# Kernel tuning notes

Measured on AMD Instinct MI355X. Metric: run time of the kernel, lower is better.

## Reference

```python
import jax, jax.numpy as jnp
import numpy as np
import math

HEAD_DIM = 128
N_HEADS = 32
N_KV_HEADS = 8
HIDDEN = 4096
ROPE_BASE = 10000.0


def _rope_cos_sin(position_ids):
    # inv_freq: [D/2]
    inv_freq = 1.0 / (ROPE_BASE ** (jnp.arange(0, HEAD_DIM, 2, dtype=jnp.float32) / HEAD_DIM))
    freqs = position_ids.astype(jnp.float32)[..., None] * inv_freq  # [B,S,D/2]
    emb = jnp.concatenate([freqs, freqs], axis=-1)  # [B,S,D]
    return jnp.cos(emb), jnp.sin(emb)


def _rotate_half(x):
    x1, x2 = jnp.split(x, 2, axis=-1)
    return jnp.concatenate([-x2, x1], axis=-1)


def setup_inputs() -> dict:
    key = jax.random.key(0)
    ks = jax.random.split(key, 5)
    B, S = 1, 2048
    inp = {
        "hidden_states": jax.random.normal(ks[0], (B, S, HIDDEN), dtype=jnp.float32),
        "position_ids": jnp.arange(B * S, dtype=jnp.int32).reshape(B, S),
        "Wq": jax.random.normal(ks[1], (HIDDEN, N_HEADS * HEAD_DIM), dtype=jnp.float32) * 0.02,
        "Wk": jax.random.normal(ks[2], (HIDDEN, N_KV_HEADS * HEAD_DIM), dtype=jnp.float32) * 0.02,
        "Wv": jax.random.normal(ks[3], (HIDDEN, N_KV_HEADS * HEAD_DIM), dtype=jnp.float32) * 0.02,
        "Wo": jax.random.normal(ks[4], (N_HEADS * HEAD_DIM, HIDDEN), dtype=jnp.float32) * 0.02,
    }
    return inp


def reference(hidden_states, position_ids, Wq, Wk, Wv, Wo):
    B, S, _ = hidden_states.shape
    G = N_HEADS // N_KV_HEADS

    q = (hidden_states @ Wq).reshape(B, S, N_HEADS, HEAD_DIM).transpose(0, 2, 1, 3)      # [B,H,S,D]
    k = (hidden_states @ Wk).reshape(B, S, N_KV_HEADS, HEAD_DIM).transpose(0, 2, 1, 3)   # [B,Hkv,S,D]
    v = (hidden_states @ Wv).reshape(B, S, N_KV_HEADS, HEAD_DIM).transpose(0, 2, 1, 3)

    cos, sin = _rope_cos_sin(position_ids)          # [B,S,D]
    cos = cos[:, None, :, :]                         # [B,1,S,D]
    sin = sin[:, None, :, :]
    q = q * cos + _rotate_half(q) * sin
    k = k * cos + _rotate_half(k) * sin

    # GQA head expansion (repeat_interleave over head dim)
    k = jnp.repeat(k, G, axis=1)                     # [B,H,S,D]
    v = jnp.repeat(v, G, axis=1)

    scale = 1.0 / math.sqrt(HEAD_DIM)
    scores = jnp.einsum("bhqd,bhkd->bhqk", q, k) * scale  # [B,H,S,S]
    causal = jnp.triu(jnp.full((S, S), -jnp.inf, dtype=scores.dtype), k=1)
    scores = scores + causal[None, None]
    probs = jax.nn.softmax(scores.astype(jnp.float32), axis=-1).astype(q.dtype)
    ctx = jnp.einsum("bhqk,bhkd->bhqd", probs, v)    # [B,H,S,D]
    ctx = ctx.transpose(0, 2, 1, 3).reshape(B, S, N_HEADS * HEAD_DIM)
    return ctx @ Wo
```

## Files before the change

kernel.cpp:

```cpp
#include <hip/hip_runtime.h>
#include <hip/hip_bf16.h>
#include <math.h>

#define SEQ 2048
#define NHEADS 32
#define NKVH 8
#define HD 128
#define HIDDEN 4096

typedef unsigned short u16;
typedef unsigned int u32;
typedef __attribute__((ext_vector_type(8))) __bf16 bf16x8;
typedef __attribute__((ext_vector_type(4))) float f32x4;
typedef __attribute__((ext_vector_type(16))) float f32x16;
typedef __attribute__((ext_vector_type(4))) u16 u16x4;
typedef __attribute__((ext_vector_type(4))) u32 u32x4;

__device__ __forceinline__ u16 f2bf(float f) {
  u32 u = __builtin_bit_cast(u32, f);
  u32 r = (u + 0x7fffu + ((u >> 16) & 1u)) >> 16;
  return (u16)r;
}
__device__ __forceinline__ float bf2f(u16 h) {
  return __builtin_bit_cast(float, ((u32)h) << 16);
}
__device__ __forceinline__ void gload_lds16(const void* g, void* l) {
  __builtin_amdgcn_global_load_lds(
      (const __attribute__((address_space(1))) u32*)g,
      (__attribute__((address_space(3))) u32*)l, 16, 0, 0);
}

#define BAR __builtin_amdgcn_s_barrier()
#define PRIO1 __builtin_amdgcn_s_setprio(1)
#define PRIO0 __builtin_amdgcn_s_setprio(0)
#define VMW(n) asm volatile("s_waitcnt vmcnt(" #n ")" ::: "memory")

__global__ void __launch_bounds__(256) conv_f2b_vec(const float* __restrict__ in,
                                                    u16* __restrict__ out, const int n) {
  const int i = (blockIdx.x * 256 + threadIdx.x) * 4;
  if (i >= n) return;
  const float4 v = *(const float4*)(in + i);
  u16x4 o;
  o.x = f2bf(v.x); o.y = f2bf(v.y); o.z = f2bf(v.z); o.w = f2bf(v.w);
  *(u16x4*)(out + i) = o;
}

__global__ void __launch_bounds__(256) trans_f2b(const float* __restrict__ in,
                                                 u16* __restrict__ out, const int R, const int C) {
  __shared__ float tile[32][33];
  const int c0 = blockIdx.x * 32, r0 = blockIdx.y * 32;
  const int tx = threadIdx.x & 31, ty = threadIdx.x >> 5;
#pragma unroll
  for (int i = 0; i < 4; ++i)
    tile[ty + i * 8][tx] = in[(size_t)(r0 + ty + i * 8) * C + c0 + tx];
  __syncthreads();
#pragma unroll
  for (int i = 0; i < 4; ++i)
    out[(size_t)(c0 + ty + i * 8) * R + r0 + tx] = f2bf(tile[tx][ty + i * 8]);
}

__global__ void __launch_bounds__(256) trans_b2b(const u16* __restrict__ in,
                                                 u16* __restrict__ out, const int R, const int C) {
  __shared__ u16 tile[32][34];
  const int c0 = blockIdx.x * 32, r0 = blockIdx.y * 32;
  const int tx = threadIdx.x & 31, ty = threadIdx.x >> 5;
#pragma unroll
  for (int i = 0; i < 4; ++i)
    tile[ty + i * 8][tx] = in[(size_t)(r0 + ty + i * 8) * C + c0 + tx];
  __syncthreads();
#pragma unroll
  for (int i = 0; i < 4; ++i)
    out[(size_t)(c0 + ty + i * 8) * R + r0 + tx] = tile[tx][ty + i * 8];
}

__global__ void __launch_bounds__(256) rope_ip(u16* __restrict__ x, const int* __restrict__ pos,
                                               const int lognh, const float oscale) {
  const int idx = blockIdx.x * 256 + threadIdx.x;
  const int j = idx & 63;
  const int hh = (idx >> 6) & ((1 << lognh) - 1);
  const int s = idx >> (6 + lognh);
  if (s >= SEQ) return;
  const float p = (float)pos[s];
  const float invf = __expf((float)j * -0.14391156831212787f);
  const float ang = p * invf;
  const float c = cosf(ang), sn = sinf(ang);
  u16* bp = x + ((size_t)s << (7 + lognh)) + hh * 128 + j;
  const float x1 = bf2f(bp[0]), x2 = bf2f(bp[64]);
  bp[0] = f2bf((x1 * c - x2 * sn) * oscale);
  bp[64] = f2bf((x2 * c + x1 * sn) * oscale);
}

template <int MH, int NH>
__device__ __forceinline__ void mfq32(f32x16 (&acc)[4][2], const bf16x8 (&afr)[2][4],
                                      const bf16x8 (&b)[4]) {
#pragma unroll
  for (int f = 0; f < 2; ++f)
#pragma unroll
    for (int ks = 0; ks < 4; ++ks)
      acc[MH * 2 + f][NH] = __builtin_amdgcn_mfma_f32_32x32x16_bf16(
          afr[f][ks], b[ks], acc[MH * 2 + f][NH], 0, 0, 0);
}

__global__ void __launch_bounds__(512, 2) gemm8p32(
    const u16* __restrict__ A, const u16* __restrict__ B0q, const u16* __restrict__ B1q,
    const u16* __restrict__ B2q, u16* __restrict__ C0, u16* __restrict__ C1,
    u16* __restrict__ C2, const float* __restrict__ Wsrc, u16* __restrict__ Wdst) {
  __shared__ u16 As[2][2][128 * 64];
  __shared__ u16 Bs[2][2][128 * 64];
  const int t = threadIdx.x;
  const int flat = blockIdx.x;
  const int swz = (flat & 7) * 32 + (flat >> 3);

  if (swz >= 192) {
    const int wid = swz - 192;
    float* tf = (float*)&As[0][0][0];
    const int tx = t & 63, ty = t >> 6;
    const int r0 = wid * 64;
    for (int ct = 0; ct < 64; ++ct) {
      const int c0 = ct * 64;
#pragma unroll
      for (int i = 0; i < 8; ++i)
        tf[(ty + i * 8) * 65 + tx] = Wsrc[(size_t)(r0 + ty + i * 8) * 4096 + c0 + tx];
      __syncthreads();
#pragma unroll
      for (int i = 0; i < 8; ++i)
        Wdst[(size_t)(c0 + ty + i * 8) * 4096 + r0 + tx] = f2bf(tf[tx * 65 + ty + i * 8]);
      __syncthreads();
    }
    return;
  }

  const int lane = t & 63, w = t >> 6;
  const int wr = w >> 2, wc = w & 3;
  const int l31 = lane & 31, l5 = lane >> 5;

  int bxt = swz % 24;
  const int byt = swz / 24;
  const u16* Bp; u16* Cw; int Nn;
  if (bxt < 16) { Bp = B0q; Cw = C0; Nn = 4096; }
  else if (bxt < 20) { bxt -= 16; Bp = B1q; Cw = C1; Nn = 1024; }
  else { bxt -= 20; Bp = B2q; Cw = C2; Nn = 1024; }
  const int row0 = byt * 256, col0 = bxt * 256;

  auto stageA = [&](int buf, int half, int tile) {
#pragma unroll
    for (int g = 0; g < 2; ++g) {
      const int o = (g * 512 + t) * 16;
      const int ridx = o >> 7;
      const int slot = (o >> 4) & 7;
      const int gr = (ridx >> 6) * 128 + half * 64 + (ridx & 63);
      gload_lds16(A + (size_t)(row0 + gr) * 4096 + (tile << 6) + ((slot ^ (ridx & 7)) << 3),
                  (char*)&As[buf][half][0] + o);
    }
  };
  auto stageB = [&](int buf, int half, int tile) {
#pragma unroll
    for (int g = 0; g < 2; ++g) {
      const int o = (g * 512 + t) * 16;
      const int ridx = o >> 7;
      const int slot = (o >> 4) & 7;
      const int gn = (ridx >> 5) * 64 + half * 32 + (ridx & 31);
      gload_lds16(Bp + (size_t)(col0 + gn) * 4096 + (tile << 6) + ((slot ^ (ridx & 7)) << 3),
                  (char*)&Bs[buf][half][0] + o);
    }
  };

  bf16x8 afr[2][4], bf0[4], bf1[4];
  auto loadA32 = [&](int buf, int half) {
#pragma unroll
    for (int f = 0; f < 2; ++f)
#pragma unroll
      for (int ks = 0; ks < 4; ++ks) {
        const int idx = wr * 64 + f * 32 + l31;
        const int slot = ks * 2 + l5;
        afr[f][ks] = *(const bf16x8*)((const char*)&As[buf][half][0] + idx * 128 +
                                      ((slot ^ (idx & 7)) << 4));
      }
  };
  auto loadB32 = [&](int buf, int half, bf16x8 (&dst)[4]) {
#pragma unroll
    for (int ks = 0; ks < 4; ++ks) {
      const int idx = wc * 32 + l31;
      const int slot = ks * 2 + l5;
      dst[ks] = *(const bf16x8*)((const char*)&Bs[buf][half][0] + idx * 128 +
                                 ((slot ^ (idx & 7)) << 4));
    }
  };

  f32x16 acc[4][2];
#pragma unroll
  for (int m_ = 0; m_ < 4; ++m_)
#pragma unroll
    for (int n_ = 0; n_ < 2; ++n_)
#pragma unroll
      for (int e = 0; e < 16; ++e) acc[m_][n_][e] = 0.f;

  const int nit = (4096 >> 6) >> 1;

  stageA(0, 0, 0); stageA(0, 1, 0); stageB(0, 0, 0); stageB(0, 1, 0);
  stageA(1, 0, 1); stageB(1, 1, 1);
  VMW(4);
  BAR;

  for (int i = 0; i < nit; ++i) {
    const int tb = 2 * i;
    const bool g2 = (i + 1 < nit);
    loadA32(0, 0); loadB32(0, 0, bf0);
    stageA(1, 1, tb + 1);
    BAR; PRIO1; mfq32<0, 0>(acc, afr, bf0); PRIO0; BAR;
    loadB32(0, 1, bf1);
    stageB(1, 0, tb + 1);
    BAR; PRIO1; mfq32<0, 1>(acc, afr, bf1); PRIO0; BAR;
    loadA32(0, 1);
    if (g2) stageA(0, 0, tb + 2);
    BAR; PRIO1; mfq32<1, 1>(acc, afr, bf1); PRIO0; BAR;
    if (g2) stageB(0, 1, tb + 2);
    BAR; PRIO1; mfq32<1, 0>(acc, afr, bf0); PRIO0;
    if (g2) { VMW(4); } else { VMW(0); }
    BAR;
    loadA32(1, 0); loadB32(1, 0, bf0);
    if (g2) stageA(0, 1, tb + 2);
    BAR; PRIO1; mfq32<0, 0>(acc, afr, bf0); PRIO0; BAR;
    loadB32(1, 1, bf1);
    if (g2) stageB(0, 0, tb + 2);
    BAR; PRIO1; mfq32<0, 1>(acc, afr, bf1); PRIO0; BAR;
    loadA32(1, 1);
    if (g2) stageA(1, 0, tb + 3);
    BAR; PRIO1; mfq32<1, 1>(acc, afr, bf1); PRIO0; BAR;
    if (g2) stageB(1, 1, tb + 3);
    BAR; PRIO1; mfq32<1, 0>(acc, afr, bf0); PRIO0;
    if (g2) { VMW(4); } else { VMW(0); }
    BAR;
  }

#pragma unroll
  for (int am = 0; am < 4; ++am)
#pragma unroll
    for (int an = 0; an < 2; ++an) {
      const int colb = col0 + wc * 64 + an * 32 + l31;
#pragma unroll
      for (int q = 0; q < 4; ++q) {
        const int rowb = row0 + wr * 128 + am * 32 + q * 8 + l5 * 4;
#pragma unroll
        for (int rr = 0; rr < 4; ++rr)
          Cw[(size_t)(rowb + rr) * Nn + colb] = f2bf(acc[am][an][q * 4 + rr]);
      }
    }
}

template <int MH, int NH>
__device__ __forceinline__ void mfq16(f32x4 (&acc)[4][4], const bf16x8 (&af)[2][2],
                                      const bf16x8 (&b)[2][2]) {
#pragma unroll
  for (int f = 0; f < 2; ++f)
#pragma unroll
    for (int e = 0; e < 2; ++e)
#pragma unroll
      for (int ks = 0; ks < 2; ++ks)
        acc[MH * 2 + f][NH * 2 + e] = __builtin_amdgcn_mfma_f32_16x16x32_bf16(
            af[f][ks], b[e][ks], acc[MH * 2 + f][NH * 2 + e], 0, 0, 0);
}

__global__ void __launch_bounds__(512, 2) gemm8p16(
    const u16* __restrict__ A, const u16* __restrict__ B, float* __restrict__ C) {
  __shared__ u16 As[2][2][64 * 64];
  __shared__ u16 Bs[2][2][128 * 64];
  const int t = threadIdx.x;
  const int lane = t & 63, w = t >> 6;
  const int wr = w >> 2, wc = w & 3;
  const int l15 = lane & 15, l4 = lane >> 4;

  const int flat = blockIdx.x;
  const int swz = (flat & 7) * 32 + (flat >> 3);
  const int bxt = swz & 15, byt = swz >> 4;
  const int row0 = byt * 128, col0 = bxt * 256;

  auto stageA = [&](int buf, int half, int tile) {
    const int o = t * 16;
    const int ridx = o >> 7;
    const int slot = (o >> 4) & 7;
    const int gr = (ridx >> 5) * 64 + half * 32 + (ridx & 31);
    gload_lds16(A + (size_t)(row0 + gr) * 4096 + (tile << 6) + ((slot ^ (ridx & 7)) << 3),
                (char*)&As[buf][half][0] + o);
  };
  auto stageB = [&](int buf, int half, int tile) {
#pragma unroll
    for (int g = 0; g < 2; ++g) {
      const int o = (g * 512 + t) * 16;
      const int ridx = o >> 7;
      const int slot = (o >> 4) & 7;
      const int gn = (ridx >> 5) * 64 + half * 32 + (ridx & 31);
      gload_lds16(B + (size_t)(col0 + gn) * 4096 + (tile << 6) + ((slot ^ (ridx & 7)) << 3),
                  (char*)&Bs[buf][half][0] + o);
    }
  };

  bf16x8 af[2][2], bf0[2][2], bf1[2][2];
  auto loadA = [&](int buf, int half) {
#pragma unroll
    for (int f = 0; f < 2; ++f)
#pragma unroll
      for (int ks = 0; ks < 2; ++ks) {
        const int idx = wr * 32 + f * 16 + l15;
        const int slot = ks * 4 + l4;
        af[f][ks] = *(const bf16x8*)((const char*)&As[buf][half][0] + idx * 128 +
                                     ((slot ^ (idx & 7)) << 4));
      }
  };
  auto loadB = [&](int buf, int half, bf16x8 (&dst)[2][2]) {
#pragma unroll
    for (int e = 0; e < 2; ++e)
#pragma unroll
      for (int ks = 0; ks < 2; ++ks) {
        const int idx = wc * 32 + e * 16 + l15;
        const int slot = ks * 4 + l4;
        dst[e][ks] = *(const bf16x8*)((const char*)&Bs[buf][half][0] + idx * 128 +
                                      ((slot ^ (idx & 7)) << 4));
      }
  };

  f32x4 acc[4][4];
#pragma unroll
  for (int m_ = 0; m_ < 4; ++m_)
#pragma unroll
    for (int n_ = 0; n_ < 4; ++n_) acc[m_][n_] = f32x4{0.f, 0.f, 0.f, 0.f};

  const int nit = (4096 >> 6) >> 1;

  stageA(0, 0, 0); stageA(0, 1, 0); stageB(0, 0, 0); stageB(0, 1, 0);
  stageA(1, 0, 1); stageB(1, 1, 1);
  VMW(3);
  BAR;

  for (int i = 0; i < nit; ++i) {
    const int tb = 2 * i;
    const bool g2 = (i + 1 < nit);
    loadA(0, 0); loadB(0, 0, bf0);
    stageA(1, 1, tb + 1);
    BAR; PRIO1; mfq16<0, 0>(acc, af, bf0); PRIO0; BAR;
    loadB(0, 1, bf1);
    stageB(1, 0, tb + 1);
    BAR; PRIO1; mfq16<0, 1>(acc, af, bf1); PRIO0; BAR;
    loadA(0, 1);
    if (g2) stageA(0, 0, tb + 2);
    BAR; PRIO1; mfq16<1, 1>(acc, af, bf1); PRIO0; BAR;
    if (g2) stageB(0, 1, tb + 2);
    BAR; PRIO1; mfq16<1, 0>(acc, af, bf0); PRIO0;
    if (g2) { VMW(3); } else { VMW(0); }
    BAR;
    loadA(1, 0); loadB(1, 0, bf0);
    if (g2) stageA(0, 1, tb + 2);
    BAR; PRIO1; mfq16<0, 0>(acc, af, bf0); PRIO0; BAR;
    loadB(1, 1, bf1);
    if (g2) stageB(0, 0, tb + 2);
    BAR; PRIO1; mfq16<0, 1>(acc, af, bf1); PRIO0; BAR;
    loadA(1, 1);
    if (g2) stageA(1, 0, tb + 3);
    BAR; PRIO1; mfq16<1, 1>(acc, af, bf1); PRIO0; BAR;
    if (g2) stageB(1, 1, tb + 3);
    BAR; PRIO1; mfq16<1, 0>(acc, af, bf0); PRIO0;
    if (g2) { VMW(3); } else { VMW(0); }
    BAR;
  }

#pragma unroll
  for (int am = 0; am < 4; ++am) {
    const int rowb = row0 + wr * 64 + (am >> 1) * 32 + (am & 1) * 16 + l4 * 4;
#pragma unroll
    for (int an = 0; an < 4; ++an) {
      const int colb = col0 + wc * 64 + (an >> 1) * 32 + (an & 1) * 16 + l15;
#pragma unroll
      for (int r = 0; r < 4; ++r)
        C[(size_t)(rowb + r) * 4096 + colb] = acc[am][an][r];
    }
  }
}

__device__ __forceinline__ void stage_kv(const u16* __restrict__ k, const u16* __restrict__ vt,
                                         const int kvh, const int kv0, u16* KsB, u16* VsB,
                                         const int t) {
#pragma unroll
  for (int i = 0; i < 4; ++i) {
    const int o = (i * 256 + t) * 16;
    const int row = o >> 8;
    const int slot = (o >> 4) & 15;
    gload_lds16(k + (size_t)(kv0 + row) * (NKVH * HD) + kvh * HD + ((slot ^ (row & 7)) << 3),
                (char*)KsB + o);
  }
#pragma unroll
  for (int i = 0; i < 4; ++i) {
    const int o = (i * 256 + t) * 16;
    const int row = o >> 7;
    const int slot = (o >> 4) & 7;
    gload_lds16(vt + (size_t)(kvh * HD + row) * SEQ + kv0 + ((slot ^ (row & 7)) << 3),
                (char*)VsB + o);
  }
}

__global__ void __launch_bounds__(256) attn_fwd(const u16* __restrict__ q, const u16* __restrict__ k,
                                                const u16* __restrict__ vt, u16* __restrict__ ctx) {
  __shared__ u16 Ks[2][64 * 128];
  __shared__ u16 Vs[2][128 * 64];
  const int t = threadIdx.x, lane = t & 63, w = t >> 6;
  const int h = blockIdx.x;
  const int qb = (int)gridDim.y - 1 - (int)blockIdx.y;
  const int kvh = h >> 2;
  const int q0 = qb * 64;
  const int sq_base = q0 + w * 16;
  const int l15 = lane & 15, l4 = lane >> 4;
  const int sq_abs = sq_base + l15;

  bf16x8 qf[4];
  {
    const u16* qp = q + (size_t)sq_abs * (NHEADS * HD) + h * HD + l4 * 8;
#pragma unroll
    for (int kb = 0; kb < 4; ++kb) qf[kb] = *(const bf16x8*)(qp + kb * 32);
  }
  f32x4 po[8];
#pragma unroll
  for (int i = 0; i < 8; ++i) po[i] = f32x4{0.f, 0.f, 0.f, 0.f};
  float mrow = -1e30f;
  float lrow = 0.f;

  const int nb = qb + 1;
  stage_kv(k, vt, kvh, 0, Ks[0], Vs[0], t);
  __syncthreads();
  int cur = 0;

  for (int b = 0; b < nb; ++b) {
    if (b + 1 < nb) stage_kv(k, vt, kvh, (b + 1) * 64, Ks[cur ^ 1], Vs[cur ^ 1], t);

    f32x4 st[4];
#pragma unroll
    for (int c = 0; c < 4; ++c) st[c] = f32x4{0.f, 0.f, 0.f, 0.f};
#pragma unroll
    for (int c = 0; c < 4; ++c) {
      const int row = c * 16 + l15;
#pragma unroll
      for (int kb = 0; kb < 4; ++kb) {
        const int slot = kb * 4 + l4;
        bf16x8 bk = *(const bf16x8*)((const char*)Ks[cur] + row * 256 + ((slot ^ (row & 7)) << 4));
        st[c] = __builtin_amdgcn_mfma_f32_16x16x32_bf16(bk, qf[kb], st[c], 0, 0, 0);
      }
    }

    if (b == nb - 1) {
#pragma unroll
      for (int c = 0; c < 4; ++c)
#pragma unroll
        for (int r = 0; r < 4; ++r) {
          const int sk = b * 64 + c * 16 + l4 * 4 + r;
          if (sk > sq_abs) st[c][r] = -1e30f;
        }
    }

    float rmax = -3e38f;
#pragma unroll
    for (int c = 0; c < 4; ++c)
      rmax = fmaxf(rmax, fmaxf(fmaxf(st[c][0], st[c][1]), fmaxf(st[c][2], st[c][3])));
    rmax = fmaxf(rmax, __shfl_xor(rmax, 16, 64));
    rmax = fmaxf(rmax, __shfl_xor(rmax, 32, 64));

    const bool skip = __all(rmax <= mrow + 8.f);
    const float mnew = skip ? mrow : fmaxf(mrow, rmax);

    float rs = 0.f;
#pragma unroll
    for (int c = 0; c < 4; ++c) {
      const float e0 = exp2f(st[c][0] - mnew), e1 = exp2f(st[c][1] - mnew);
      const float e2 = exp2f(st[c][2] - mnew), e3 = exp2f(st[c][3] - mnew);
      st[c][0] = e0; st[c][1] = e1; st[c][2] = e2; st[c][3] = e3;
      rs += (e0 + e1) + (e2 + e3);
    }
    rs += __shfl_xor(rs, 16, 64);
    rs += __shfl_xor(rs, 32, 64);

    if (!skip) {
      const float alpha = exp2f(mrow - mnew);
      mrow = mnew;
      lrow = lrow * alpha + rs;
      float av[4];
#pragma unroll
      for (int r = 0; r < 4; ++r) av[r] = __shfl(alpha, l4 * 4 + r, 16);
#pragma unroll
      for (int db = 0; db < 8; ++db)
#pragma unroll
        for (int r = 0; r < 4; ++r) po[db][r] *= av[r];
    } else {
      lrow += rs;
    }

    u32 pk[4][2];
#pragma unroll
    for (int c = 0; c < 4; ++c) {
      pk[c][0] = (u32)f2bf(st[c][0]) | ((u32)f2bf(st[c][1]) << 16);
      pk[c][1] = (u32)f2bf(st[c][2]) | ((u32)f2bf(st[c][3]) << 16);
    }
    const int src01 = l15 + ((lane & 16) << 1);
    const int src23 = src01 + 16;
    const bool lo = (lane & 32) == 0;
#pragma unroll
    for (int kb2 = 0; kb2 < 2; ++kb2) {
      const int c0 = kb2 * 2, c1 = c0 + 1;
      const u32 a0 = (u32)__shfl((int)pk[c0][0], src01, 64);
      const u32 a1 = (u32)__shfl((int)pk[c0][1], src01, 64);
      const u32 a2 = (u32)__shfl((int)pk[c0][0], src23, 64);
      const u32 a3 = (u32)__shfl((int)pk[c0][1], src23, 64);
      const u32 b0 = (u32)__shfl((int)pk[c1][0], src01, 64);
      const u32 b1 = (u32)__shfl((int)pk[c1][1], src01, 64);
      const u32 b2 = (u32)__shfl((int)pk[c1][0], src23, 64);
      const u32 b3 = (u32)__shfl((int)pk[c1][1], src23, 64);
      u32x4 wq;
      wq.x = lo ? a0 : b0;
      wq.y = lo ? a1 : b1;
      wq.z = lo ? a2 : b2;
      wq.w = lo ? a3 : b3;
      const bf16x8 pa = __builtin_bit_cast(bf16x8, wq);
#pragma unroll
      for (int db = 0; db < 8; ++db) {
        const int vrow = db * 16 + l15;
        const int pslot = kb2 * 4 + l4;
        bf16x8 bv = *(const bf16x8*)((const char*)Vs[cur] + vrow * 128 + ((pslot ^ (vrow & 7)) << 4));
        po[db] = __builtin_amdgcn_mfma_f32_16x16x32_bf16(pa, bv, po[db], 0, 0, 0);
      }
    }
    __syncthreads();
    cur ^= 1;
  }

  float rl[4];
#pragma unroll
  for (int r = 0; r < 4; ++r) rl[r] = 1.f / __shfl(lrow, l4 * 4 + r, 16);
#pragma unroll
  for (int db = 0; db < 8; ++db)
#pragma unroll
    for (int r = 0; r < 4; ++r) {
      const int sq = sq_base + l4 * 4 + r;
      const int d = db * 16 + l15;
      ctx[(size_t)sq * (NHEADS * HD) + h * HD + d] = f2bf(po[db][r] * rl[r]);
    }
}

extern "C" void kernel_launch(void* const* d_in, const int* in_sizes, int n_in,
                              void* d_out, int out_size, void* d_ws, size_t ws_size,
                              hipStream_t stream) {
  const float* hs = (const float*)d_in[0];
  const int* pos = (const int*)d_in[1];
  const float* Wq = (const float*)d_in[2];
  const float* Wk = (const float*)d_in[3];
  const float* Wv = (const float*)d_in[4];
  const float* Wo = (const float*)d_in[5];

  u16* ws = (u16*)d_ws;
  u16* Xb = ws;
  u16* Wqt = Xb + (size_t)2048 * 4096;
  u16* Wkt = Wqt + (size_t)4096 * 4096;
  u16* Wvt = Wkt + (size_t)1024 * 4096;
  u16* Wot = Wvt + (size_t)1024 * 4096;
  u16* qb = Wot + (size_t)4096 * 4096;
  u16* kb = qb + (size_t)2048 * 4096;
  u16* vb = kb + (size_t)2048 * 1024;
  u16* vtb = vb + (size_t)2048 * 1024;
  u16* ctx = vtb + (size_t)1024 * 2048;
  const size_t need = ((size_t)(ctx - ws) + (size_t)2048 * 4096) * 2;
  if (ws_size < need) return;

  conv_f2b_vec<<<8192, 256, 0, stream>>>(hs, Xb, 2048 * 4096);
  trans_f2b<<<dim3(128, 128), 256, 0, stream>>>(Wq, Wqt, 4096, 4096);
  trans_f2b<<<dim3(32, 128), 256, 0, stream>>>(Wk, Wkt, 4096, 1024);
  trans_f2b<<<dim3(32, 128), 256, 0, stream>>>(Wv, Wvt, 4096, 1024);

  gemm8p32<<<256, 512, 0, stream>>>(Xb, Wqt, Wkt, Wvt, qb, kb, vb, Wo, Wot);

  const float qscale = 0.08838834764831845f * 1.44269504088896340f;
  rope_ip<<<16384, 256, 0, stream>>>(qb, pos, 5, qscale);
  rope_ip<<<4096, 256, 0, stream>>>(kb, pos, 3, 1.0f);

  trans_b2b<<<dim3(32, 64), 256, 0, stream>>>(vb, vtb, 2048, 1024);

  attn_fwd<<<dim3(32, 32), 256, 0, stream>>>(qb, kb, vtb, ctx);

  gemm8p16<<<256, 512, 0, stream>>>(ctx, Wot, (float*)d_out);
}
```

Measured before the change: 351.5 us.

## Restructure GEMM main loops for register-prefetched fragments and fuse prep kernels

Both 8-phase GEMM kernels now double-buffer the register fragments for A and B (even/odd sets). Each phase loads the fragments for the next MFMA block while the current one runs, and the last iteration is peeled into a separate tail. The goal is to hide LDS read latency behind MFMA work and drop the per-iteration conditional staging. Separately, the four input-preparation launches (hidden-state conversion plus three weight transposes) are merged into one kernel with 64x64 transpose tiles, which cuts launch overhead. The cost is higher register pressure and the extra vmcnt waits now placed in every phase.

```diff
diff --git a/kernel.cpp b/kernel.cpp
--- a/kernel.cpp
+++ b/kernel.cpp
@@ -35,42 +35,35 @@
 #define PRIO0 __builtin_amdgcn_s_setprio(0)
 #define VMW(n) asm volatile("s_waitcnt vmcnt(" #n ")" ::: "memory")
 
-__global__ void __launch_bounds__(256) conv_f2b_vec(const float* __restrict__ in,
-                                                    u16* __restrict__ out, const int n) {
-  const int i = (blockIdx.x * 256 + threadIdx.x) * 4;
-  if (i >= n) return;
-  const float4 v = *(const float4*)(in + i);
-  u16x4 o;
-  o.x = f2bf(v.x); o.y = f2bf(v.y); o.z = f2bf(v.z); o.w = f2bf(v.w);
-  *(u16x4*)(out + i) = o;
-}
-
-__global__ void __launch_bounds__(256) trans_f2b(const float* __restrict__ in,
-                                                 u16* __restrict__ out, const int R, const int C) {
-  __shared__ float tile[32][33];
-  const int c0 = blockIdx.x * 32, r0 = blockIdx.y * 32;
-  const int tx = threadIdx.x & 31, ty = threadIdx.x >> 5;
-#pragma unroll
-  for (int i = 0; i < 4; ++i)
-    tile[ty + i * 8][tx] = in[(size_t)(r0 + ty + i * 8) * C + c0 + tx];
+__global__ void __launch_bounds__(256) prep_all(
+    const float* __restrict__ hs, u16* __restrict__ Xb,
+    const float* __restrict__ Wq, u16* __restrict__ Wqt,
+    const float* __restrict__ Wk, u16* __restrict__ Wkt,
+    const float* __restrict__ Wv, u16* __restrict__ Wvt) {
+  const int bid = blockIdx.x;
+  if (bid < 8192) {
+    const int i = (bid * 256 + threadIdx.x) * 4;
+    const float4 v = *(const float4*)(hs + i);
+    u16x4 o;
+    o.x = f2bf(v.x); o.y = f2bf(v.y); o.z = f2bf(v.z); o.w = f2bf(v.w);
+    *(u16x4*)(Xb + i) = o;
+    return;
+  }
+  __shared__ float tile[64][65];
+  const float* src; u16* dst; int C, lc, tb;
+  const int b2 = bid - 8192;
+  if (b2 < 4096) { src = Wq; dst = Wqt; C = 4096; lc = 6; tb = b2; }
+  else if (b2 < 5120) { src = Wk; dst = Wkt; C = 1024; lc = 4; tb = b2 - 4096; }
+  else { src = Wv; dst = Wvt; C = 1024; lc = 4; tb = b2 - 5120; }
+  const int r0 = (tb >> lc) * 64, c0 = (tb & ((1 << lc) - 1)) * 64;
+  const int tx = threadIdx.x & 63, ty = threadIdx.x >> 6;
+#pragma unroll
+  for (int j = 0; j < 16; ++j)
+    tile[ty + j * 4][tx] = src[(size_t)(r0 + ty + j * 4) * C + c0 + tx];
   __syncthreads();
 #pragma unroll
-  for (int i = 0; i < 4; ++i)
-    out[(size_t)(c0 + ty + i * 8) * R + r0 + tx] = f2bf(tile[tx][ty + i * 8]);
-}
-
-__global__ void __launch_bounds__(256) trans_b2b(const u16* __restrict__ in,
-                                                 u16* __restrict__ out, const int R, const int C) {
-  __shared__ u16 tile[32][34];
-  const int c0 = blockIdx.x * 32, r0 = blockIdx.y * 32;
-  const int tx = threadIdx.x & 31, ty = threadIdx.x >> 5;
-#pragma unroll
-  for (int i = 0; i < 4; ++i)
-    tile[ty + i * 8][tx] = in[(size_t)(r0 + ty + i * 8) * C + c0 + tx];
-  __syncthreads();
-#pragma unroll
-  for (int i = 0; i < 4; ++i)
-    out[(size_t)(c0 + ty + i * 8) * R + r0 + tx] = tile[tx][ty + i * 8];
+  for (int j = 0; j < 16; ++j)
+    dst[(size_t)(c0 + ty + j * 4) * 4096 + r0 + tx] = f2bf(tile[tx][ty + j * 4]);
 }
 
 __global__ void __launch_bounds__(256) rope_ip(u16* __restrict__ x, const int* __restrict__ pos,
@@ -90,6 +83,20 @@
   bp[64] = f2bf((x2 * c + x1 * sn) * oscale);
 }
 
+__global__ void __launch_bounds__(256) trans_b2b(const u16* __restrict__ in,
+                                                 u16* __restrict__ out, const int R, const int C) {
+  __shared__ u16 tile[32][34];
+  const int c0 = blockIdx.x * 32, r0 = blockIdx.y * 32;
+  const int tx = threadIdx.x & 31, ty = threadIdx.x >> 5;
+#pragma unroll
+  for (int i = 0; i < 4; ++i)
+    tile[ty + i * 8][tx] = in[(size_t)(r0 + ty + i * 8) * C + c0 + tx];
+  __syncthreads();
+#pragma unroll
+  for (int i = 0; i < 4; ++i)
+    out[(size_t)(c0 + ty + i * 8) * R + r0 + tx] = tile[tx][ty + i * 8];
+}
+
 template <int MH, int NH>
 __device__ __forceinline__ void mfq32(f32x16 (&acc)[4][2], const bf16x8 (&afr)[2][4],
                                       const bf16x8 (&b)[4]) {
@@ -165,17 +172,15 @@
     }
   };
 
-  bf16x8 afr[2][4], bf0[4], bf1[4];
-  auto loadA32 = [&](int buf, int half) {
-#pragma unroll
-    for (int f = 0; f < 2; ++f)
-#pragma unroll
-      for (int ks = 0; ks < 4; ++ks) {
-        const int idx = wr * 64 + f * 32 + l31;
-        const int slot = ks * 2 + l5;
-        afr[f][ks] = *(const bf16x8*)((const char*)&As[buf][half][0] + idx * 128 +
-                                      ((slot ^ (idx & 7)) << 4));
-      }
+  bf16x8 aE[2][4], aO[2][4], bX[4], bY[4];
+  auto loadAf = [&](int buf, int half, int f, bf16x8 (&dst)[4]) {
+#pragma unroll
+    for (int ks = 0; ks < 4; ++ks) {
+      const int idx = wr * 64 + f * 32 + l31;
+      const int slot = ks * 2 + l5;
+      dst[ks] = *(const bf16x8*)((const char*)&As[buf][half][0] + idx * 128 +
+                                 ((slot ^ (idx & 7)) << 4));
+    }
   };
   auto loadB32 = [&](int buf, int half, bf16x8 (&dst)[4]) {
 #pragma unroll
@@ -197,41 +202,61 @@
 
   const int nit = (4096 >> 6) >> 1;
 
-  stageA(0, 0, 0); stageA(0, 1, 0); stageB(0, 0, 0); stageB(0, 1, 0);
-  stageA(1, 0, 1); stageB(1, 1, 1);
-  VMW(4);
+  stageA(0, 0, 0); stageB(0, 0, 0); stageA(0, 1, 0); stageB(0, 1, 0);
+  stageA(1, 0, 1); stageB(1, 0, 1); stageA(1, 1, 1); stageB(1, 1, 1);
+  VMW(6);
   BAR;
-
-  for (int i = 0; i < nit; ++i) {
+  loadAf(0, 0, 0, aE[0]); loadAf(0, 0, 1, aE[1]); loadB32(0, 0, bX);
+  BAR;
+
+  for (int i = 0; i < nit - 1; ++i) {
     const int tb = 2 * i;
-    const bool g2 = (i + 1 < nit);
-    loadA32(0, 0); loadB32(0, 0, bf0);
-    stageA(1, 1, tb + 1);
-    BAR; PRIO1; mfq32<0, 0>(acc, afr, bf0); PRIO0; BAR;
-    loadB32(0, 1, bf1);
-    stageB(1, 0, tb + 1);
-    BAR; PRIO1; mfq32<0, 1>(acc, afr, bf1); PRIO0; BAR;
-    loadA32(0, 1);
-    if (g2) stageA(0, 0, tb + 2);
-    BAR; PRIO1; mfq32<1, 1>(acc, afr, bf1); PRIO0; BAR;
-    if (g2) stageB(0, 1, tb + 2);
-    BAR; PRIO1; mfq32<1, 0>(acc, afr, bf0); PRIO0;
-    if (g2) { VMW(4); } else { VMW(0); }
-    BAR;
-    loadA32(1, 0); loadB32(1, 0, bf0);
-    if (g2) stageA(0, 1, tb + 2);
-    BAR; PRIO1; mfq32<0, 0>(acc, afr, bf0); PRIO0; BAR;
-    loadB32(1, 1, bf1);
-    if (g2) stageB(0, 0, tb + 2);
-    BAR; PRIO1; mfq32<0, 1>(acc, afr, bf1); PRIO0; BAR;
-    loadA32(1, 1);
-    if (g2) stageA(1, 0, tb + 3);
-    BAR; PRIO1; mfq32<1, 1>(acc, afr, bf1); PRIO0; BAR;
-    if (g2) stageB(1, 1, tb + 3);
-    BAR; PRIO1; mfq32<1, 0>(acc, afr, bf0); PRIO0;
-    if (g2) { VMW(4); } else { VMW(0); }
-    BAR;
-  }
+    loadAf(0, 1, 0, aO[0]); loadB32(0, 1, bY);
+    stageA(0, 0, tb + 2);
+    BAR; PRIO1; mfq32<0, 0>(acc, aE, bX); PRIO0; VMW(6); BAR;
+    loadAf(0, 1, 1, aO[1]);
+    stageB(0, 0, tb + 2);
+    BAR; PRIO1; mfq32<0, 1>(acc, aE, bY); PRIO0; VMW(6); BAR;
+    loadAf(1, 0, 0, aE[0]);
+    stageA(0, 1, tb + 2);
+    BAR; PRIO1; mfq32<1, 1>(acc, aO, bY); PRIO0; VMW(6); BAR;
+    loadAf(1, 0, 1, aE[1]); loadB32(1, 0, bY);
+    stageB(0, 1, tb + 2);
+    BAR; PRIO1; mfq32<1, 0>(acc, aO, bX); PRIO0; VMW(6); BAR;
+    loadAf(1, 1, 0, aO[0]); loadB32(1, 1, bX);
+    stageA(1, 0, tb + 3);
+    BAR; PRIO1; mfq32<0, 0>(acc, aE, bY); PRIO0; VMW(6); BAR;
+    loadAf(1, 1, 1, aO[1]);
+    stageB(1, 0, tb + 3);
+    BAR; PRIO1; mfq32<0, 1>(acc, aE, bX); PRIO0; VMW(6); BAR;
+    loadAf(0, 0, 0, aE[0]);
+    stageA(1, 1, tb + 3);
+    BAR; PRIO1; mfq32<1, 1>(acc, aO, bX); PRIO0; VMW(6); BAR;
+    loadAf(0, 0, 1, aE[1]); loadB32(0, 0, bX);
+    stageB(1, 1, tb + 3);
+    BAR; PRIO1; mfq32<1, 0>(acc, aO, bY); PRIO0; VMW(6); BAR;
+  }
+
+  VMW(0);
+  BAR;
+  loadAf(0, 1, 0, aO[0]); loadAf(0, 1, 1, aO[1]); loadB32(0, 1, bY);
+  PRIO1;
+  mfq32<0, 0>(acc, aE, bX);
+  mfq32<0, 1>(acc, aE, bY);
+  PRIO0;
+  loadAf(1, 0, 0, aE[0]); loadAf(1, 0, 1, aE[1]);
+  PRIO1;
+  mfq32<1, 1>(acc, aO, bY);
+  mfq32<1, 0>(acc, aO, bX);
+  PRIO0;
+  loadB32(1, 0, bY); loadB32(1, 1, bX);
+  loadAf(1, 1, 0, aO[0]); loadAf(1, 1, 1, aO[1]);
+  PRIO1;
+  mfq32<0, 0>(acc, aE, bY);
+  mfq32<0, 1>(acc, aE, bX);
+  mfq32<1, 1>(acc, aO, bX);
+  mfq32<1, 0>(acc, aO, bY);
+  PRIO0;
 
 #pragma unroll
   for (int am = 0; am < 4; ++am)
@@ -295,19 +320,17 @@
     }
   };
 
-  bf16x8 af[2][2], bf0[2][2], bf1[2][2];
-  auto loadA = [&](int buf, int half) {
-#pragma unroll
-    for (int f = 0; f < 2; ++f)
-#pragma unroll
-      for (int ks = 0; ks < 2; ++ks) {
-        const int idx = wr * 32 + f * 16 + l15;
-        const int slot = ks * 4 + l4;
-        af[f][ks] = *(const bf16x8*)((const char*)&As[buf][half][0] + idx * 128 +
-                                     ((slot ^ (idx & 7)) << 4));
-      }
-  };
-  auto loadB = [&](int buf, int half, bf16x8 (&dst)[2][2]) {
+  bf16x8 aE[2][2], aO[2][2], bX[2][2], bY[2][2];
+  auto loadAf = [&](int buf, int half, int f, bf16x8 (&dst)[2]) {
+#pragma unroll
+    for (int ks = 0; ks < 2; ++ks) {
+      const int idx = wr * 32 + f * 16 + l15;
+      const int slot = ks * 4 + l4;
+      dst[ks] = *(const bf16x8*)((const char*)&As[buf][half][0] + idx * 128 +
+                                 ((slot ^ (idx & 7)) << 4));
+    }
+  };
+  auto loadB16 = [&](int buf, int half, bf16x8 (&dst)[2][2]) {
 #pragma unroll
     for (int e = 0; e < 2; ++e)
 #pragma unroll
@@ -327,41 +350,61 @@
 
   const int nit = (4096 >> 6) >> 1;
 
-  stageA(0, 0, 0); stageA(0, 1, 0); stageB(0, 0, 0); stageB(0, 1, 0);
-  stageA(1, 0, 1); stageB(1, 1, 1);
-  VMW(3);
+  stageA(0, 0, 0); stageB(0, 0, 0); stageA(0, 1, 0); stageB(0, 1, 0);
+  stageA(1, 0, 1); stageB(1, 0, 1); stageA(1, 1, 1); stageB(1, 1, 1);
+  VMW(5);
   BAR;
-
-  for (int i = 0; i < nit; ++i) {
+  loadAf(0, 0, 0, aE[0]); loadAf(0, 0, 1, aE[1]); loadB16(0, 0, bX);
+  BAR;
+
+  for (int i = 0; i < nit - 1; ++i) {
     const int tb = 2 * i;
-    const bool g2 = (i + 1 < nit);
-    loadA(0, 0); loadB(0, 0, bf0);
-    stageA(1, 1, tb + 1);
-    BAR; PRIO1; mfq16<0, 0>(acc, af, bf0); PRIO0; BAR;
-    loadB(0, 1, bf1);
-    stageB(1, 0, tb + 1);
-    BAR; PRIO1; mfq16<0, 1>(acc, af, bf1); PRIO0; BAR;
-    loadA(0, 1);
-    if (g2) stageA(0, 0, tb + 2);
-    BAR; PRIO1; mfq16<1, 1>(acc, af, bf1); PRIO0; BAR;
-    if (g2) stageB(0, 1, tb + 2);
-    BAR; PRIO1; mfq16<1, 0>(acc, af, bf0); PRIO0;
-    if (g2) { VMW(3); } else { VMW(0); }
-    BAR;
-    loadA(1, 0); loadB(1, 0, bf0);
-    if (g2) stageA(0, 1, tb + 2);
-    BAR; PRIO1; mfq16<0, 0>(acc, af, bf0); PRIO0; BAR;
-    loadB(1, 1, bf1);
-    if (g2) stageB(0, 0, tb + 2);
-    BAR; PRIO1; mfq16<0, 1>(acc, af, bf1); PRIO0; BAR;
-    loadA(1, 1);
-    if (g2) stageA(1, 0, tb + 3);
-    BAR; PRIO1; mfq16<1, 1>(acc, af, bf1); PRIO0; BAR;
-    if (g2) stageB(1, 1, tb + 3);
-    BAR; PRIO1; mfq16<1, 0>(acc, af, bf0); PRIO0;
-    if (g2) { VMW(3); } else { VMW(0); }
-    BAR;
-  }
+    loadAf(0, 1, 0, aO[0]); loadB16(0, 1, bY);
+    stageA(0, 0, tb + 2);
+    BAR; PRIO1; mfq16<0, 0>(acc, aE, bX); PRIO0; VMW(4); BAR;
+    loadAf(0, 1, 1, aO[1]);
+    stageB(0, 0, tb + 2);
+    BAR; PRIO1; mfq16<0, 1>(acc, aE, bY); PRIO0; VMW(4); BAR;
+    loadAf(1, 0, 0, aE[0]);
+    stageA(0, 1, tb + 2);
+    BAR; PRIO1; mfq16<1, 1>(acc, aO, bY); PRIO0; VMW(4); BAR;
+    loadAf(1, 0, 1, aE[1]); loadB16(1, 0, bY);
+    stageB(0, 1, tb + 2);
+    BAR; PRIO1; mfq16<1, 0>(acc, aO, bX); PRIO0; VMW(4); BAR;
+    loadAf(1, 1, 0, aO[0]); loadB16(1, 1, bX);
+    stageA(1, 0, tb + 3);
+    BAR; PRIO1; mfq16<0, 0>(acc, aE, bY); PRIO0; VMW(4); BAR;
+    loadAf(1, 1, 1, aO[1]);
+    stageB(1, 0, tb + 3);
+    BAR; PRIO1; mfq16<0, 1>(acc, aE, bX); PRIO0; VMW(4); BAR;
+    loadAf(0, 0, 0, aE[0]);
+    stageA(1, 1, tb + 3);
+    BAR; PRIO1; mfq16<1, 1>(acc, aO, bX); PRIO0; VMW(4); BAR;
+    loadAf(0, 0, 1, aE[1]); loadB16(0, 0, bX);
+    stageB(1, 1, tb + 3);
+    BAR; PRIO1; mfq16<1, 0>(acc, aO, bY); PRIO0; VMW(4); BAR;
+  }
+
+  VMW(0);
+  BAR;
+  loadAf(0, 1, 0, aO[0]); loadAf(0, 1, 1, aO[1]); loadB16(0, 1, bY);
+  PRIO1;
+  mfq16<0, 0>(acc, aE, bX);
+  mfq16<0, 1>(acc, aE, bY);
+  PRIO0;
+  loadAf(1, 0, 0, aE[0]); loadAf(1, 0, 1, aE[1]);
+  PRIO1;
+  mfq16<1, 1>(acc, aO, bY);
+  mfq16<1, 0>(acc, aO, bX);
+  PRIO0;
+  loadB16(1, 0, bY); loadB16(1, 1, bX);
+  loadAf(1, 1, 0, aO[0]); loadAf(1, 1, 1, aO[1]);
+  PRIO1;
+  mfq16<0, 0>(acc, aE, bY);
+  mfq16<0, 1>(acc, aE, bX);
+  mfq16<1, 1>(acc, aO, bX);
+  mfq16<1, 0>(acc, aO, bY);
+  PRIO0;
 
 #pragma unroll
   for (int am = 0; am < 4; ++am) {
@@ -565,10 +608,7 @@
   const size_t need = ((size_t)(ctx - ws) + (size_t)2048 * 4096) * 2;
   if (ws_size < need) return;
 
-  conv_f2b_vec<<<8192, 256, 0, stream>>>(hs, Xb, 2048 * 4096);
-  trans_f2b<<<dim3(128, 128), 256, 0, stream>>>(Wq, Wqt, 4096, 4096);
-  trans_f2b<<<dim3(32, 128), 256, 0, stream>>>(Wk, Wkt, 4096, 1024);
-  trans_f2b<<<dim3(32, 128), 256, 0, stream>>>(Wv, Wvt, 4096, 1024);
+  prep_all<<<14336, 256, 0, stream>>>(hs, Xb, Wq, Wqt, Wk, Wkt, Wv, Wvt);
 
   gemm8p32<<<256, 512, 0, stream>>>(Xb, Wqt, Wkt, Wvt, qb, kb, vb, Wo, Wot);
 
```

After: 411.1 us. 1.17x slower.

## Merge prep and post-QKV kernels, deepen GEMM prefetch to two stages ahead

Applied to the files above, without the earlier changes.

Four preprocessing launches (hidden-state cast plus three weight transposes) become one multi-role kernel with 64x64 transpose tiles. The two RoPE launches and the V transpose are likewise fused into a single kernel, cutting launch count and tail gaps. In both GEMMs the staging schedule changes so a whole k-tile pair is issued ahead, with deeper vmcnt waits (8/6). This keeps more global loads in flight, at the risk of more outstanding memory pressure and subtle ordering bugs in the last-iteration wait.

```diff
diff --git a/kernel.cpp b/kernel.cpp
--- a/kernel.cpp
+++ b/kernel.cpp
@@ -35,59 +35,77 @@
 #define PRIO0 __builtin_amdgcn_s_setprio(0)
 #define VMW(n) asm volatile("s_waitcnt vmcnt(" #n ")" ::: "memory")
 
-__global__ void __launch_bounds__(256) conv_f2b_vec(const float* __restrict__ in,
-                                                    u16* __restrict__ out, const int n) {
-  const int i = (blockIdx.x * 256 + threadIdx.x) * 4;
-  if (i >= n) return;
-  const float4 v = *(const float4*)(in + i);
-  u16x4 o;
-  o.x = f2bf(v.x); o.y = f2bf(v.y); o.z = f2bf(v.z); o.w = f2bf(v.w);
-  *(u16x4*)(out + i) = o;
-}
-
-__global__ void __launch_bounds__(256) trans_f2b(const float* __restrict__ in,
-                                                 u16* __restrict__ out, const int R, const int C) {
-  __shared__ float tile[32][33];
-  const int c0 = blockIdx.x * 32, r0 = blockIdx.y * 32;
+__global__ void __launch_bounds__(256) prep_all(
+    const float* __restrict__ hs, u16* __restrict__ Xb,
+    const float* __restrict__ Wq, u16* __restrict__ Wqt,
+    const float* __restrict__ Wk, u16* __restrict__ Wkt,
+    const float* __restrict__ Wv, u16* __restrict__ Wvt) {
+  const int bid = blockIdx.x;
+  if (bid < 8192) {
+    const int i = (bid * 256 + threadIdx.x) * 4;
+    const float4 v = *(const float4*)(hs + i);
+    u16x4 o;
+    o.x = f2bf(v.x); o.y = f2bf(v.y); o.z = f2bf(v.z); o.w = f2bf(v.w);
+    *(u16x4*)(Xb + i) = o;
+    return;
+  }
+  __shared__ float tile[64][65];
+  const float* src; u16* dst; int C, lc, tb;
+  const int b2 = bid - 8192;
+  if (b2 < 4096) { src = Wq; dst = Wqt; C = 4096; lc = 6; tb = b2; }
+  else if (b2 < 5120) { src = Wk; dst = Wkt; C = 1024; lc = 4; tb = b2 - 4096; }
+  else { src = Wv; dst = Wvt; C = 1024; lc = 4; tb = b2 - 5120; }
+  const int r0 = (tb >> lc) * 64, c0 = (tb & ((1 << lc) - 1)) * 64;
+  const int tx = threadIdx.x & 63, ty = threadIdx.x >> 6;
+#pragma unroll
+  for (int j = 0; j < 16; ++j)
+    tile[ty + j * 4][tx] = src[(size_t)(r0 + ty + j * 4) * C + c0 + tx];
+  __syncthreads();
+#pragma unroll
+  for (int j = 0; j < 16; ++j)
+    dst[(size_t)(c0 + ty + j * 4) * 4096 + r0 + tx] = f2bf(tile[tx][ty + j * 4]);
+}
+
+__global__ void __launch_bounds__(256) post_qkv(u16* __restrict__ qb, u16* __restrict__ kb,
+                                                const u16* __restrict__ vb, u16* __restrict__ vtb,
+                                                const int* __restrict__ pos) {
+  const int bid = blockIdx.x;
+  if (bid < 20480) {
+    u16* x; int lognh; float oscale;
+    int idx;
+    if (bid < 16384) {
+      x = qb; lognh = 5;
+      oscale = 0.08838834764831845f * 1.44269504088896340f;
+      idx = bid * 256 + threadIdx.x;
+    } else {
+      x = kb; lognh = 3; oscale = 1.0f;
+      idx = (bid - 16384) * 256 + threadIdx.x;
+    }
+    const int j = idx & 63;
+    const int hh = (idx >> 6) & ((1 << lognh) - 1);
+    const int s = idx >> (6 + lognh);
+    if (s >= SEQ) return;
+    const float p = (float)pos[s];
+    const float invf = __expf((float)j * -0.14391156831212787f);
+    const float ang = p * invf;
+    const float c = cosf(ang), sn = sinf(ang);
+    u16* bp = x + ((size_t)s << (7 + lognh)) + hh * 128 + j;
+    const float x1 = bf2f(bp[0]), x2 = bf2f(bp[64]);
+    bp[0] = f2bf((x1 * c - x2 * sn) * oscale);
+    bp[64] = f2bf((x2 * c + x1 * sn) * oscale);
+    return;
+  }
+  __shared__ u16 tile[32][34];
+  const int b2 = bid - 20480;
+  const int c0 = (b2 & 31) * 32, r0 = (b2 >> 5) * 32;
   const int tx = threadIdx.x & 31, ty = threadIdx.x >> 5;
 #pragma unroll
   for (int i = 0; i < 4; ++i)
-    tile[ty + i * 8][tx] = in[(size_t)(r0 + ty + i * 8) * C + c0 + tx];
+    tile[ty + i * 8][tx] = vb[(size_t)(r0 + ty + i * 8) * 1024 + c0 + tx];
   __syncthreads();
 #pragma unroll
   for (int i = 0; i < 4; ++i)
-    out[(size_t)(c0 + ty + i * 8) * R + r0 + tx] = f2bf(tile[tx][ty + i * 8]);
-}
-
-__global__ void __launch_bounds__(256) trans_b2b(const u16* __restrict__ in,
-                                                 u16* __restrict__ out, const int R, const int C) {
-  __shared__ u16 tile[32][34];
-  const int c0 = blockIdx.x * 32, r0 = blockIdx.y * 32;
-  const int tx = threadIdx.x & 31, ty = threadIdx.x >> 5;
-#pragma unroll
-  for (int i = 0; i < 4; ++i)
-    tile[ty + i * 8][tx] = in[(size_t)(r0 + ty + i * 8) * C + c0 + tx];
-  __syncthreads();
-#pragma unroll
-  for (int i = 0; i < 4; ++i)
-    out[(size_t)(c0 + ty + i * 8) * R + r0 + tx] = tile[tx][ty + i * 8];
-}
-
-__global__ void __launch_bounds__(256) rope_ip(u16* __restrict__ x, const int* __restrict__ pos,
-                                               const int lognh, const float oscale) {
-  const int idx = blockIdx.x * 256 + threadIdx.x;
-  const int j = idx & 63;
-  const int hh = (idx >> 6) & ((1 << lognh) - 1);
-  const int s = idx >> (6 + lognh);
-  if (s >= SEQ) return;
-  const float p = (float)pos[s];
-  const float invf = __expf((float)j * -0.14391156831212787f);
-  const float ang = p * invf;
-  const float c = cosf(ang), sn = sinf(ang);
-  u16* bp = x + ((size_t)s << (7 + lognh)) + hh * 128 + j;
-  const float x1 = bf2f(bp[0]), x2 = bf2f(bp[64]);
-  bp[0] = f2bf((x1 * c - x2 * sn) * oscale);
-  bp[64] = f2bf((x2 * c + x1 * sn) * oscale);
+    vtb[(size_t)(c0 + ty + i * 8) * 2048 + r0 + tx] = tile[tx][ty + i * 8];
 }
 
 template <int MH, int NH>
@@ -197,39 +215,37 @@
 
   const int nit = (4096 >> 6) >> 1;
 
-  stageA(0, 0, 0); stageA(0, 1, 0); stageB(0, 0, 0); stageB(0, 1, 0);
-  stageA(1, 0, 1); stageB(1, 1, 1);
-  VMW(4);
+  stageA(0, 0, 0); stageB(0, 0, 0); stageB(0, 1, 0); stageA(0, 1, 0);
+  stageA(1, 0, 1); stageB(1, 0, 1); stageB(1, 1, 1); stageA(1, 1, 1);
+  VMW(8);
   BAR;
 
   for (int i = 0; i < nit; ++i) {
     const int tb = 2 * i;
     const bool g2 = (i + 1 < nit);
     loadA32(0, 0); loadB32(0, 0, bf0);
-    stageA(1, 1, tb + 1);
     BAR; PRIO1; mfq32<0, 0>(acc, afr, bf0); PRIO0; BAR;
     loadB32(0, 1, bf1);
-    stageB(1, 0, tb + 1);
+    if (g2) { stageA(0, 0, tb + 2); stageB(0, 0, tb + 2); }
     BAR; PRIO1; mfq32<0, 1>(acc, afr, bf1); PRIO0; BAR;
     loadA32(0, 1);
-    if (g2) stageA(0, 0, tb + 2);
+    if (g2) stageB(0, 1, tb + 2);
     BAR; PRIO1; mfq32<1, 1>(acc, afr, bf1); PRIO0; BAR;
-    if (g2) stageB(0, 1, tb + 2);
+    if (g2) stageA(0, 1, tb + 2);
     BAR; PRIO1; mfq32<1, 0>(acc, afr, bf0); PRIO0;
-    if (g2) { VMW(4); } else { VMW(0); }
+    if (g2) { VMW(8); } else { VMW(0); }
     BAR;
     loadA32(1, 0); loadB32(1, 0, bf0);
-    if (g2) stageA(0, 1, tb + 2);
     BAR; PRIO1; mfq32<0, 0>(acc, afr, bf0); PRIO0; BAR;
     loadB32(1, 1, bf1);
-    if (g2) stageB(0, 0, tb + 2);
+    if (g2) { stageA(1, 0, tb + 3); stageB(1, 0, tb + 3); }
     BAR; PRIO1; mfq32<0, 1>(acc, afr, bf1); PRIO0; BAR;
     loadA32(1, 1);
-    if (g2) stageA(1, 0, tb + 3);
+    if (g2) stageB(1, 1, tb + 3);
     BAR; PRIO1; mfq32<1, 1>(acc, afr, bf1); PRIO0; BAR;
-    if (g2) stageB(1, 1, tb + 3);
+    if (g2) stageA(1, 1, tb + 3);
     BAR; PRIO1; mfq32<1, 0>(acc, afr, bf0); PRIO0;
-    if (g2) { VMW(4); } else { VMW(0); }
+    if (g2) { VMW(8); } else { }
     BAR;
   }
 
@@ -327,39 +343,37 @@
 
   const int nit = (4096 >> 6) >> 1;
 
-  stageA(0, 0, 0); stageA(0, 1, 0); stageB(0, 0, 0); stageB(0, 1, 0);
-  stageA(1, 0, 1); stageB(1, 1, 1);
-  VMW(3);
+  stageA(0, 0, 0); stageB(0, 0, 0); stageB(0, 1, 0); stageA(0, 1, 0);
+  stageA(1, 0, 1); stageB(1, 0, 1); stageB(1, 1, 1); stageA(1, 1, 1);
+  VMW(6);
   BAR;
 
   for (int i = 0; i < nit; ++i) {
     const int tb = 2 * i;
     const bool g2 = (i + 1 < nit);
     loadA(0, 0); loadB(0, 0, bf0);
-    stageA(1, 1, tb + 1);
     BAR; PRIO1; mfq16<0, 0>(acc, af, bf0); PRIO0; BAR;
     loadB(0, 1, bf1);
-    stageB(1, 0, tb + 1);
+    if (g2) { stageA(0, 0, tb + 2); stageB(0, 0, tb + 2); }
     BAR; PRIO1; mfq16<0, 1>(acc, af, bf1); PRIO0; BAR;
     loadA(0, 1);
-    if (g2) stageA(0, 0, tb + 2);
+    if (g2) stageB(0, 1, tb + 2);
     BAR; PRIO1; mfq16<1, 1>(acc, af, bf1); PRIO0; BAR;
-    if (g2) stageB(0, 1, tb + 2);
+    if (g2) stageA(0, 1, tb + 2);
     BAR; PRIO1; mfq16<1, 0>(acc, af, bf0); PRIO0;
-    if (g2) { VMW(3); } else { VMW(0); }
+    if (g2) { VMW(6); } else { VMW(0); }
     BAR;
     loadA(1, 0); loadB(1, 0, bf0);
-    if (g2) stageA(0, 1, tb + 2);
     BAR; PRIO1; mfq16<0, 0>(acc, af, bf0); PRIO0; BAR;
     loadB(1, 1, bf1);
-    if (g2) stageB(0, 0, tb + 2);
+    if (g2) { stageA(1, 0, tb + 3); stageB(1, 0, tb + 3); }
     BAR; PRIO1; mfq16<0, 1>(acc, af, bf1); PRIO0; BAR;
     loadA(1, 1);
-    if (g2) stageA(1, 0, tb + 3);
+    if (g2) stageB(1, 1, tb + 3);
     BAR; PRIO1; mfq16<1, 1>(acc, af, bf1); PRIO0; BAR;
-    if (g2) stageB(1, 1, tb + 3);
+    if (g2) stageA(1, 1, tb + 3);
     BAR; PRIO1; mfq16<1, 0>(acc, af, bf0); PRIO0;
-    if (g2) { VMW(3); } else { VMW(0); }
+    if (g2) { VMW(6); } else { }
     BAR;
   }
 
@@ -565,18 +579,11 @@
   const size_t need = ((size_t)(ctx - ws) + (size_t)2048 * 4096) * 2;
   if (ws_size < need) return;
 
-  conv_f2b_vec<<<8192, 256, 0, stream>>>(hs, Xb, 2048 * 4096);
-  trans_f2b<<<dim3(128, 128), 256, 0, stream>>>(Wq, Wqt, 4096, 4096);
-  trans_f2b<<<dim3(32, 128), 256, 0, stream>>>(Wk, Wkt, 4096, 1024);
-  trans_f2b<<<dim3(32, 128), 256, 0, stream>>>(Wv, Wvt, 4096, 1024);
+  prep_all<<<14336, 256, 0, stream>>>(hs, Xb, Wq, Wqt, Wk, Wkt, Wv, Wvt);
 
   gemm8p32<<<256, 512, 0, stream>>>(Xb, Wqt, Wkt, Wvt, qb, kb, vb, Wo, Wot);
 
-  const float qscale = 0.08838834764831845f * 1.44269504088896340f;
-  rope_ip<<<16384, 256, 0, stream>>>(qb, pos, 5, qscale);
-  rope_ip<<<4096, 256, 0, stream>>>(kb, pos, 3, 1.0f);
-
-  trans_b2b<<<dim3(32, 64), 256, 0, stream>>>(vb, vtb, 2048, 1024);
+  post_qkv<<<22528, 256, 0, stream>>>(qb, kb, vb, vtb, pos);
 
   attn_fwd<<<dim3(32, 32), 256, 0, stream>>>(qb, kb, vtb, ctx);
 
```

New measurement: 346.4 us. No clear change (-1.5%).
